# Optimization experiments

Hardware: AMD Instinct MI355X
Metric: run time of the kernel (lower is better)

## Reference

```python
import jax, jax.numpy as jnp
import numpy as np

B, TE, TD, H = 4, 1024, 512, 128


def setup_inputs() -> dict:
    key = jax.random.key(0)
    k1, k2, k3, k4, k5 = jax.random.split(key, 5)
    return {
        "encoder_out": jax.random.normal(k1, (B, TE, H), dtype=jnp.float32),
        "decoder_out": jax.random.normal(k2, (B, TD, H), dtype=jnp.float32),
        "W_a": jax.random.normal(k3, (H, H), dtype=jnp.float32) * 0.05,
        "U_a": jax.random.normal(k4, (H, H), dtype=jnp.float32) * 0.05,
        "V_a": jax.random.normal(k5, (H, 1), dtype=jnp.float32) * 0.05,
    }


def reference(encoder_out, decoder_out, W_a, U_a, V_a):
    # Bahdanau additive attention, vectorized over all decoder steps at once.
    # (The original K.rnn loop has no true recurrence; steps are independent.)
    W_s = jnp.einsum('bth,hk->btk', encoder_out, W_a)   # [B, Te, H]
    U_h = jnp.einsum('bdh,hk->bdk', decoder_out, U_a)   # [B, Td, H]
    # energies: v^T tanh(W s_t + U h_d) -> [B, Td, Te]
    tanh_arg = jnp.tanh(W_s[:, None, :, :] + U_h[:, :, None, :])  # [B, Td, Te, H]
    e = jnp.einsum('bdth,ho->bdt', tanh_arg, V_a)
    e = jax.nn.softmax(e, axis=-1)                      # attention weights [B, Td, Te]
    # context vectors: weighted sum over encoder positions -> [B, Td, H]
    c = jnp.einsum('bdt,bth->bdh', e, encoder_out)
    return (c, e)
```

## Files before the change

### kernel.cpp

```cpp
#include <hip/hip_runtime.h>

#define BB    4
#define TE    1024
#define TD    512
#define HH    128
#define DTILE 4
#define TTILE 64
#define LOG2E 1.4426950408889634f

__device__ __forceinline__ void gload16_lds(const float* g, float* l) {
    __builtin_amdgcn_global_load_lds(
        (const __attribute__((address_space(1))) unsigned int*)g,
        (__attribute__((address_space(3))) unsigned int*)l, 16, 0, 0);
}

__device__ __forceinline__ float tanhsum4(float4 A, float4 B, float4 v, float acc) {
    acc = fmaf(v.x * (A.x + B.x), __builtin_amdgcn_rcpf(fmaf(A.x, B.x, 1.0f)), acc);
    acc = fmaf(v.y * (A.y + B.y), __builtin_amdgcn_rcpf(fmaf(A.y, B.y, 1.0f)), acc);
    acc = fmaf(v.z * (A.z + B.z), __builtin_amdgcn_rcpf(fmaf(A.z, B.z, 1.0f)), acc);
    acc = fmaf(v.w * (A.w + B.w), __builtin_amdgcn_rcpf(fmaf(A.w, B.w, 1.0f)), acc);
    return acc;
}

__device__ __forceinline__ float tanh_eval(float x) {
    float e = __builtin_amdgcn_exp2f(2.0f * LOG2E * x);
    return 1.0f - 2.0f * __builtin_amdgcn_rcpf(e + 1.0f);
}

__global__ __launch_bounds__(256) void proj_gemm(
    const float* __restrict__ enc, const float* __restrict__ dec,
    const float* __restrict__ Wa,  const float* __restrict__ Ua,
    float* __restrict__ out)
{
    __shared__ float Xs[64 * 33];
    __shared__ float Ws[32 * 64];

    const int tid = threadIdx.x;
    const int rt = blockIdx.x >> 1, ch = blockIdx.x & 1;
    const int r0 = rt * 64, c0 = ch * 64;

    const float* X; const float* W; int rX0;
    if (r0 < BB * TE) { X = enc; W = Wa; rX0 = r0; }
    else              { X = dec; W = Ua; rX0 = r0 - BB * TE; }

    const int c4 = tid & 15;
    const int rg = tid >> 4;

    float4 a0 = {0,0,0,0}, a1 = a0, a2 = a0, a3 = a0;

    for (int kc = 0; kc < 4; ++kc) {
        #pragma unroll
        for (int i = 0; i < 2; ++i) {
            int idx = tid + i * 256;
            int r  = idx >> 3, k4 = idx & 7;
            *(float4*)&Xs[r * 33 + k4 * 4] =
                *(const float4*)&X[(rX0 + r) * HH + kc * 32 + k4 * 4];
            int kk = idx >> 4, cc = idx & 15;
            *(float4*)&Ws[kk * 64 + cc * 4] =
                *(const float4*)&W[(kc * 32 + kk) * HH + c0 + cc * 4];
        }
        __syncthreads();
        #pragma unroll 8
        for (int k = 0; k < 32; ++k) {
            float4 wv = *(const float4*)&Ws[k * 64 + c4 * 4];
            float x0 = Xs[(rg * 4 + 0) * 33 + k];
            float x1 = Xs[(rg * 4 + 1) * 33 + k];
            float x2 = Xs[(rg * 4 + 2) * 33 + k];
            float x3 = Xs[(rg * 4 + 3) * 33 + k];
            a0.x = fmaf(x0, wv.x, a0.x); a0.y = fmaf(x0, wv.y, a0.y);
            a0.z = fmaf(x0, wv.z, a0.z); a0.w = fmaf(x0, wv.w, a0.w);
            a1.x = fmaf(x1, wv.x, a1.x); a1.y = fmaf(x1, wv.y, a1.y);
            a1.z = fmaf(x1, wv.z, a1.z); a1.w = fmaf(x1, wv.w, a1.w);
            a2.x = fmaf(x2, wv.x, a2.x); a2.y = fmaf(x2, wv.y, a2.y);
            a2.z = fmaf(x2, wv.z, a2.z); a2.w = fmaf(x2, wv.w, a2.w);
            a3.x = fmaf(x3, wv.x, a3.x); a3.y = fmaf(x3, wv.y, a3.y);
            a3.z = fmaf(x3, wv.z, a3.z); a3.w = fmaf(x3, wv.w, a3.w);
        }
        __syncthreads();
    }

    float4 accs[4] = {a0, a1, a2, a3};
    #pragma unroll
    for (int j = 0; j < 4; ++j) {
        float4 o = accs[j];
        o.x = tanh_eval(o.x); o.y = tanh_eval(o.y);
        o.z = tanh_eval(o.z); o.w = tanh_eval(o.w);
        *(float4*)&out[(r0 + rg * 4 + j) * HH + c0 + c4 * 4] = o;
    }
}

__global__ __launch_bounds__(512, 4) void attn_fused(
    const float* __restrict__ enc,
    const float* __restrict__ ta,
    const float* __restrict__ tb,
    const float* __restrict__ Va,
    float* __restrict__ c_out,
    float* __restrict__ e_out)
{
    __shared__ float tile[8 * 2048];
    __shared__ float e_s[DTILE * TE];

    const int tid = threadIdx.x;
    const int l   = tid & 63;
    const int w   = tid >> 6;
    const int b   = blockIdx.x >> 7;
    const int d0  = (blockIdx.x & 127) * DTILE;

    const int c8 = l & 7;
    const int r8 = l >> 3;

    float* slab = &tile[w * 2048];

    float4 B4[DTILE][4], v4[4];
    #pragma unroll
    for (int j = 0; j < 4; ++j) {
        v4[j] = *(const float4*)&Va[(j * 8 + c8) * 4];
        #pragma unroll
        for (int d = 0; d < DTILE; ++d)
            B4[d][j] = *(const float4*)&tb[((size_t)b * TD + d0 + d) * HH + (j * 8 + c8) * 4];
    }

    const float* ta_w  = ta  + (size_t)b * TE * HH + w * 8 * HH;
    const float* enc_w = enc + (size_t)b * TE * HH + w * 8 * HH;

    auto p1c = [&](int tt, const float* buf) {
        float acc[DTILE] = {0.f, 0.f, 0.f, 0.f};
        #pragma unroll
        for (int j = 0; j < 4; ++j) {
            float4 A = *(const float4*)&buf[r8 * HH + (j * 8 + c8) * 4];
            #pragma unroll
            for (int d = 0; d < DTILE; ++d)
                acc[d] = tanhsum4(A, B4[d][j], v4[j], acc[d]);
        }
        #pragma unroll
        for (int d = 0; d < DTILE; ++d) {
            acc[d] += __shfl_xor(acc[d], 1);
            acc[d] += __shfl_xor(acc[d], 2);
            acc[d] += __shfl_xor(acc[d], 4);
        }
        if (c8 == 0) {
            #pragma unroll
            for (int d = 0; d < DTILE; ++d)
                e_s[d * TE + tt * TTILE + w * 8 + r8] = acc[d];
        }
    };

    #pragma unroll
    for (int i = 0; i < 4; ++i)
        gload16_lds(ta_w + i * 256 + l * 4, slab + i * 256);

    for (int tt = 0; tt < 15; ++tt) {
        const float* src = ta_w + (size_t)(tt + 1) * TTILE * HH;
        float* nb = slab + ((tt + 1) & 1) * 1024;
        #pragma unroll
        for (int i = 0; i < 4; ++i)
            gload16_lds(src + i * 256 + l * 4, nb + i * 256);
        __builtin_amdgcn_s_waitcnt(0x0F74);
        p1c(tt, slab + (tt & 1) * 1024);
        __builtin_amdgcn_sched_barrier(0);
    }
    __builtin_amdgcn_s_waitcnt(0x0F70);
    p1c(15, slab + 1024);

    __syncthreads();

    {
        const int d2 = w & 3, hf = w >> 2;
        float ev[16];
        float m = -3.0e38f;
        #pragma unroll
        for (int i = 0; i < 16; ++i) {
            ev[i] = e_s[d2 * TE + i * 64 + l];
            m = fmaxf(m, ev[i]);
        }
        #pragma unroll
        for (int off = 32; off; off >>= 1) m = fmaxf(m, __shfl_xor(m, off));
        float s = 0.f;
        #pragma unroll
        for (int i = 0; i < 16; ++i) {
            ev[i] = __builtin_amdgcn_exp2f((ev[i] - m) * LOG2E);
            s += ev[i];
        }
        #pragma unroll
        for (int off = 32; off; off >>= 1) s += __shfl_xor(s, off);
        float inv = __builtin_amdgcn_rcpf(s);

        __syncthreads();
        float* eo = e_out + ((size_t)b * TD + d0 + d2) * TE;
        #pragma unroll
        for (int i = 0; i < 8; ++i) {
            int ii = hf * 8 + i;
            float p = ev[ii] * inv;
            e_s[d2 * TE + ii * 64 + l] = p;
            eo[ii * 64 + l] = p;
        }
        __syncthreads();
    }

    const int h4 = l & 31, tsub = l >> 5;
    float4 acc4[DTILE];
    #pragma unroll
    for (int d = 0; d < DTILE; ++d) acc4[d] = make_float4(0.f, 0.f, 0.f, 0.f);

    auto p3c = [&](int tt, const float* buf) {
        float4 ep[DTILE];
        #pragma unroll
        for (int d = 0; d < DTILE; ++d)
            ep[d] = *(const float4*)&e_s[d * TE + tt * TTILE + w * 8 + tsub * 4];
        #pragma unroll
        for (int k = 0; k < 4; ++k) {
            float4 x = *(const float4*)&buf[(tsub * 4 + k) * HH + h4 * 4];
            float p0 = k == 0 ? ep[0].x : k == 1 ? ep[0].y : k == 2 ? ep[0].z : ep[0].w;
            float p1 = k == 0 ? ep[1].x : k == 1 ? ep[1].y : k == 2 ? ep[1].z : ep[1].w;
            float p2 = k == 0 ? ep[2].x : k == 1 ? ep[2].y : k == 2 ? ep[2].z : ep[2].w;
            float p3 = k == 0 ? ep[3].x : k == 1 ? ep[3].y : k == 2 ? ep[3].z : ep[3].w;
            acc4[0].x = fmaf(p0, x.x, acc4[0].x); acc4[0].y = fmaf(p0, x.y, acc4[0].y);
            acc4[0].z = fmaf(p0, x.z, acc4[0].z); acc4[0].w = fmaf(p0, x.w, acc4[0].w);
            acc4[1].x = fmaf(p1, x.x, acc4[1].x); acc4[1].y = fmaf(p1, x.y, acc4[1].y);
            acc4[1].z = fmaf(p1, x.z, acc4[1].z); acc4[1].w = fmaf(p1, x.w, acc4[1].w);
            acc4[2].x = fmaf(p2, x.x, acc4[2].x); acc4[2].y = fmaf(p2, x.y, acc4[2].y);
            acc4[2].z = fmaf(p2, x.z, acc4[2].z); acc4[2].w = fmaf(p2, x.w, acc4[2].w);
            acc4[3].x = fmaf(p3, x.x, acc4[3].x); acc4[3].y = fmaf(p3, x.y, acc4[3].y);
            acc4[3].z = fmaf(p3, x.z, acc4[3].z); acc4[3].w = fmaf(p3, x.w, acc4[3].w);
        }
    };

    #pragma unroll
    for (int i = 0; i < 4; ++i)
        gload16_lds(enc_w + i * 256 + l * 4, slab + i * 256);

    for (int tt = 0; tt < 15; ++tt) {
        const float* src = enc_w + (size_t)(tt + 1) * TTILE * HH;
        float* nb = slab + ((tt + 1) & 1) * 1024;
        #pragma unroll
        for (int i = 0; i < 4; ++i)
            gload16_lds(src + i * 256 + l * 4, nb + i * 256);
        __builtin_amdgcn_s_waitcnt(0x0F74);
        p3c(tt, slab + (tt & 1) * 1024);
        __builtin_amdgcn_sched_barrier(0);
    }
    __builtin_amdgcn_s_waitcnt(0x0F70);
    p3c(15, slab + 1024);

    #pragma unroll
    for (int d = 0; d < DTILE; ++d) {
        acc4[d].x += __shfl_xor(acc4[d].x, 32);
        acc4[d].y += __shfl_xor(acc4[d].y, 32);
        acc4[d].z += __shfl_xor(acc4[d].z, 32);
        acc4[d].w += __shfl_xor(acc4[d].w, 32);
    }
    __syncthreads();
    float* c_red = tile;
    if (tsub == 0) {
        #pragma unroll
        for (int d = 0; d < DTILE; ++d)
            *(float4*)&c_red[(w * DTILE + d) * HH + h4 * 4] = acc4[d];
    }
    __syncthreads();

    if (w < DTILE && l < 32) {
        float4 o = make_float4(0.f, 0.f, 0.f, 0.f);
        #pragma unroll
        for (int ww = 0; ww < 8; ++ww) {
            float4 p = *(const float4*)&c_red[(ww * DTILE + w) * HH + l * 4];
            o.x += p.x; o.y += p.y; o.z += p.z; o.w += p.w;
        }
        *(float4*)&c_out[((size_t)b * TD + d0 + w) * HH + l * 4] = o;
    }
}

extern "C" void kernel_launch(void* const* d_in, const int* in_sizes, int n_in,
                              void* d_out, int out_size, void* d_ws, size_t ws_size,
                              hipStream_t stream) {
    (void)in_sizes; (void)n_in; (void)out_size; (void)ws_size;

    const float* enc = (const float*)d_in[0];
    const float* dec = (const float*)d_in[1];
    const float* Wa  = (const float*)d_in[2];
    const float* Ua  = (const float*)d_in[3];
    const float* Va  = (const float*)d_in[4];

    float* c_out = (float*)d_out;
    float* e_out = (float*)d_out + BB * TD * HH;

    float* proj = (float*)d_ws;
    float* ta_p = proj;
    float* tb_p = proj + BB * TE * HH;

    proj_gemm<<<192, 256, 0, stream>>>(enc, dec, Wa, Ua, proj);
    attn_fused<<<(BB * TD) / DTILE, 512, 0, stream>>>(enc, ta_p, tb_p, Va, c_out, e_out);
}
```

Baseline: 137.7 us.

## Batch tanh-sum reciprocals via rational combination and load tiles directly into registers

Energy computation combines eight tanh-addition terms into a single numerator/denominator pair so only one reciprocal is needed per energy, reducing transcendental work. Global-to-LDS staging of the tanh and encoder tiles is replaced by register double-buffered global loads, freeing most of the shared memory. The reduction shuffle spans 16 lanes instead of 8. Risks include more register pressure, uncoalesced or latency-exposed loads without LDS staging, and slight precision changes from products of denominators.

```diff
diff --git a/kernel.cpp b/kernel.cpp
--- a/kernel.cpp
+++ b/kernel.cpp
@@ -8,23 +8,21 @@
 #define TTILE 64
 #define LOG2E 1.4426950408889634f
 
-__device__ __forceinline__ void gload16_lds(const float* g, float* l) {
-    __builtin_amdgcn_global_load_lds(
-        (const __attribute__((address_space(1))) unsigned int*)g,
-        (__attribute__((address_space(3))) unsigned int*)l, 16, 0, 0);
-}
-
-__device__ __forceinline__ float tanhsum4(float4 A, float4 B, float4 v, float acc) {
-    acc = fmaf(v.x * (A.x + B.x), __builtin_amdgcn_rcpf(fmaf(A.x, B.x, 1.0f)), acc);
-    acc = fmaf(v.y * (A.y + B.y), __builtin_amdgcn_rcpf(fmaf(A.y, B.y, 1.0f)), acc);
-    acc = fmaf(v.z * (A.z + B.z), __builtin_amdgcn_rcpf(fmaf(A.z, B.z, 1.0f)), acc);
-    acc = fmaf(v.w * (A.w + B.w), __builtin_amdgcn_rcpf(fmaf(A.w, B.w, 1.0f)), acc);
-    return acc;
-}
-
 __device__ __forceinline__ float tanh_eval(float x) {
     float e = __builtin_amdgcn_exp2f(2.0f * LOG2E * x);
     return 1.0f - 2.0f * __builtin_amdgcn_rcpf(e + 1.0f);
+}
+
+__device__ __forceinline__ void quad_nd(float4 A, float4 B, float4 v,
+                                        float& n, float& den) {
+    float n0 = v.x * (A.x + B.x), d0 = fmaf(A.x, B.x, 1.0f);
+    float n1 = v.y * (A.y + B.y), d1 = fmaf(A.y, B.y, 1.0f);
+    float n2 = v.z * (A.z + B.z), d2 = fmaf(A.z, B.z, 1.0f);
+    float n3 = v.w * (A.w + B.w), d3 = fmaf(A.w, B.w, 1.0f);
+    float n01 = fmaf(n0, d1, n1 * d0), d01 = d0 * d1;
+    float n23 = fmaf(n2, d3, n3 * d2), d23 = d2 * d3;
+    n   = fmaf(n01, d23, n23 * d01);
+    den = d01 * d23;
 }
 
 __global__ __launch_bounds__(256) void proj_gemm(
@@ -97,8 +95,8 @@
     float* __restrict__ c_out,
     float* __restrict__ e_out)
 {
-    __shared__ float tile[8 * 2048];
     __shared__ float e_s[DTILE * TE];
+    __shared__ float c_red[8 * DTILE * HH];
 
     const int tid = threadIdx.x;
     const int l   = tid & 63;
@@ -106,62 +104,66 @@
     const int b   = blockIdx.x >> 7;
     const int d0  = (blockIdx.x & 127) * DTILE;
 
-    const int c8 = l & 7;
-    const int r8 = l >> 3;
-
-    float* slab = &tile[w * 2048];
-
-    float4 B4[DTILE][4], v4[4];
-    #pragma unroll
-    for (int j = 0; j < 4; ++j) {
-        v4[j] = *(const float4*)&Va[(j * 8 + c8) * 4];
+    const int c16 = l & 15;
+    const int r4  = l >> 4;
+
+    float4 B4[DTILE][2], v4[2];
+    #pragma unroll
+    for (int j = 0; j < 2; ++j) {
+        v4[j] = *(const float4*)&Va[(j * 16 + c16) * 4];
         #pragma unroll
         for (int d = 0; d < DTILE; ++d)
-            B4[d][j] = *(const float4*)&tb[((size_t)b * TD + d0 + d) * HH + (j * 8 + c8) * 4];
-    }
-
-    const float* ta_w  = ta  + (size_t)b * TE * HH + w * 8 * HH;
-    const float* enc_w = enc + (size_t)b * TE * HH + w * 8 * HH;
-
-    auto p1c = [&](int tt, const float* buf) {
-        float acc[DTILE] = {0.f, 0.f, 0.f, 0.f};
-        #pragma unroll
-        for (int j = 0; j < 4; ++j) {
-            float4 A = *(const float4*)&buf[r8 * HH + (j * 8 + c8) * 4];
-            #pragma unroll
-            for (int d = 0; d < DTILE; ++d)
-                acc[d] = tanhsum4(A, B4[d][j], v4[j], acc[d]);
-        }
-        #pragma unroll
-        for (int d = 0; d < DTILE; ++d) {
-            acc[d] += __shfl_xor(acc[d], 1);
-            acc[d] += __shfl_xor(acc[d], 2);
-            acc[d] += __shfl_xor(acc[d], 4);
-        }
-        if (c8 == 0) {
-            #pragma unroll
-            for (int d = 0; d < DTILE; ++d)
-                e_s[d * TE + tt * TTILE + w * 8 + r8] = acc[d];
-        }
-    };
-
-    #pragma unroll
-    for (int i = 0; i < 4; ++i)
-        gload16_lds(ta_w + i * 256 + l * 4, slab + i * 256);
-
-    for (int tt = 0; tt < 15; ++tt) {
-        const float* src = ta_w + (size_t)(tt + 1) * TTILE * HH;
-        float* nb = slab + ((tt + 1) & 1) * 1024;
-        #pragma unroll
-        for (int i = 0; i < 4; ++i)
-            gload16_lds(src + i * 256 + l * 4, nb + i * 256);
-        __builtin_amdgcn_s_waitcnt(0x0F74);
-        p1c(tt, slab + (tt & 1) * 1024);
-        __builtin_amdgcn_sched_barrier(0);
-    }
-    __builtin_amdgcn_s_waitcnt(0x0F70);
-    p1c(15, slab + 1024);
-
+            B4[d][j] = *(const float4*)&tb[((size_t)b * TD + d0 + d) * HH + (j * 16 + c16) * 4];
+    }
+
+    const float* ta_w  = ta  + ((size_t)b * TE + w * 8) * HH;
+    const float* enc_w = enc + ((size_t)b * TE + w * 8) * HH;
+
+    {
+        float4 A0[2][2], A1[2][2];
+
+        auto loadA = [&](int tt, float4 (&A)[2][2]) {
+            const float* base = ta_w + (size_t)tt * TTILE * HH;
+            #pragma unroll
+            for (int hf = 0; hf < 2; ++hf)
+                #pragma unroll
+                for (int j = 0; j < 2; ++j)
+                    A[hf][j] = *(const float4*)&base[(hf * 4 + r4) * HH + (j * 16 + c16) * 4];
+        };
+
+        auto p1c = [&](int tt, float4 (&A)[2][2]) {
+            #pragma unroll
+            for (int hf = 0; hf < 2; ++hf) {
+                #pragma unroll
+                for (int d = 0; d < DTILE; ++d) {
+                    float na, da, nb, db;
+                    quad_nd(A[hf][0], B4[d][0], v4[0], na, da);
+                    quad_nd(A[hf][1], B4[d][1], v4[1], nb, db);
+                    float num = fmaf(na, db, nb * da);
+                    float den = da * db;
+                    float e = num * __builtin_amdgcn_rcpf(den);
+                    e += __shfl_xor(e, 1);
+                    e += __shfl_xor(e, 2);
+                    e += __shfl_xor(e, 4);
+                    e += __shfl_xor(e, 8);
+                    if (c16 == 0)
+                        e_s[d * TE + tt * TTILE + w * 8 + hf * 4 + r4] = e;
+                }
+            }
+        };
+
+        loadA(0, A0);
+        #pragma unroll 1
+        for (int tt = 0; tt < 14; tt += 2) {
+            loadA(tt + 1, A1);
+            p1c(tt, A0);
+            loadA(tt + 2, A0);
+            p1c(tt + 1, A1);
+        }
+        loadA(15, A1);
+        p1c(14, A0);
+        p1c(15, A1);
+    }
     __syncthreads();
 
     {
@@ -202,45 +204,51 @@
     #pragma unroll
     for (int d = 0; d < DTILE; ++d) acc4[d] = make_float4(0.f, 0.f, 0.f, 0.f);
 
-    auto p3c = [&](int tt, const float* buf) {
-        float4 ep[DTILE];
-        #pragma unroll
-        for (int d = 0; d < DTILE; ++d)
-            ep[d] = *(const float4*)&e_s[d * TE + tt * TTILE + w * 8 + tsub * 4];
-        #pragma unroll
-        for (int k = 0; k < 4; ++k) {
-            float4 x = *(const float4*)&buf[(tsub * 4 + k) * HH + h4 * 4];
-            float p0 = k == 0 ? ep[0].x : k == 1 ? ep[0].y : k == 2 ? ep[0].z : ep[0].w;
-            float p1 = k == 0 ? ep[1].x : k == 1 ? ep[1].y : k == 2 ? ep[1].z : ep[1].w;
-            float p2 = k == 0 ? ep[2].x : k == 1 ? ep[2].y : k == 2 ? ep[2].z : ep[2].w;
-            float p3 = k == 0 ? ep[3].x : k == 1 ? ep[3].y : k == 2 ? ep[3].z : ep[3].w;
-            acc4[0].x = fmaf(p0, x.x, acc4[0].x); acc4[0].y = fmaf(p0, x.y, acc4[0].y);
-            acc4[0].z = fmaf(p0, x.z, acc4[0].z); acc4[0].w = fmaf(p0, x.w, acc4[0].w);
-            acc4[1].x = fmaf(p1, x.x, acc4[1].x); acc4[1].y = fmaf(p1, x.y, acc4[1].y);
-            acc4[1].z = fmaf(p1, x.z, acc4[1].z); acc4[1].w = fmaf(p1, x.w, acc4[1].w);
-            acc4[2].x = fmaf(p2, x.x, acc4[2].x); acc4[2].y = fmaf(p2, x.y, acc4[2].y);
-            acc4[2].z = fmaf(p2, x.z, acc4[2].z); acc4[2].w = fmaf(p2, x.w, acc4[2].w);
-            acc4[3].x = fmaf(p3, x.x, acc4[3].x); acc4[3].y = fmaf(p3, x.y, acc4[3].y);
-            acc4[3].z = fmaf(p3, x.z, acc4[3].z); acc4[3].w = fmaf(p3, x.w, acc4[3].w);
-        }
-    };
-
-    #pragma unroll
-    for (int i = 0; i < 4; ++i)
-        gload16_lds(enc_w + i * 256 + l * 4, slab + i * 256);
-
-    for (int tt = 0; tt < 15; ++tt) {
-        const float* src = enc_w + (size_t)(tt + 1) * TTILE * HH;
-        float* nb = slab + ((tt + 1) & 1) * 1024;
-        #pragma unroll
-        for (int i = 0; i < 4; ++i)
-            gload16_lds(src + i * 256 + l * 4, nb + i * 256);
-        __builtin_amdgcn_s_waitcnt(0x0F74);
-        p3c(tt, slab + (tt & 1) * 1024);
-        __builtin_amdgcn_sched_barrier(0);
-    }
-    __builtin_amdgcn_s_waitcnt(0x0F70);
-    p3c(15, slab + 1024);
+    {
+        float4 X0[4], X1[4];
+
+        auto loadX = [&](int tt, float4 (&X)[4]) {
+            const float* base = enc_w + (size_t)tt * TTILE * HH;
+            #pragma unroll
+            for (int k = 0; k < 4; ++k)
+                X[k] = *(const float4*)&base[(tsub * 4 + k) * HH + h4 * 4];
+        };
+
+        auto p3c = [&](int tt, float4 (&X)[4]) {
+            float4 ep[DTILE];
+            #pragma unroll
+            for (int d = 0; d < DTILE; ++d)
+                ep[d] = *(const float4*)&e_s[d * TE + tt * TTILE + w * 8 + tsub * 4];
+            #pragma unroll
+            for (int k = 0; k < 4; ++k) {
+                float4 x = X[k];
+                float p0 = k == 0 ? ep[0].x : k == 1 ? ep[0].y : k == 2 ? ep[0].z : ep[0].w;
+                float p1 = k == 0 ? ep[1].x : k == 1 ? ep[1].y : k == 2 ? ep[1].z : ep[1].w;
+                float p2 = k == 0 ? ep[2].x : k == 1 ? ep[2].y : k == 2 ? ep[2].z : ep[2].w;
+                float p3 = k == 0 ? ep[3].x : k == 1 ? ep[3].y : k == 2 ? ep[3].z : ep[3].w;
+                acc4[0].x = fmaf(p0, x.x, acc4[0].x); acc4[0].y = fmaf(p0, x.y, acc4[0].y);
+                acc4[0].z = fmaf(p0, x.z, acc4[0].z); acc4[0].w = fmaf(p0, x.w, acc4[0].w);
+                acc4[1].x = fmaf(p1, x.x, acc4[1].x); acc4[1].y = fmaf(p1, x.y, acc4[1].y);
+                acc4[1].z = fmaf(p1, x.z, acc4[1].z); acc4[1].w = fmaf(p1, x.w, acc4[1].w);
+                acc4[2].x = fmaf(p2, x.x, acc4[2].x); acc4[2].y = fmaf(p2, x.y, acc4[2].y);
+                acc4[2].z = fmaf(p2, x.z, acc4[2].z); acc4[2].w = fmaf(p2, x.w, acc4[2].w);
+                acc4[3].x = fmaf(p3, x.x, acc4[3].x); acc4[3].y = fmaf(p3, x.y, acc4[3].y);
+                acc4[3].z = fmaf(p3, x.z, acc4[3].z); acc4[3].w = fmaf(p3, x.w, acc4[3].w);
+            }
+        };
+
+        loadX(0, X0);
+        #pragma unroll 1
+        for (int tt = 0; tt < 14; tt += 2) {
+            loadX(tt + 1, X1);
+            p3c(tt, X0);
+            loadX(tt + 2, X0);
+            p3c(tt + 1, X1);
+        }
+        loadX(15, X1);
+        p3c(14, X0);
+        p3c(15, X1);
+    }
 
     #pragma unroll
     for (int d = 0; d < DTILE; ++d) {
@@ -249,8 +257,6 @@
         acc4[d].z += __shfl_xor(acc4[d].z, 32);
         acc4[d].w += __shfl_xor(acc4[d].w, 32);
     }
-    __syncthreads();
-    float* c_red = tile;
     if (tsub == 0) {
         #pragma unroll
         for (int d = 0; d < DTILE; ++d)
```

New measurement: 125.8 us. 1.09x faster.
